# Performance work log

Hardware: AMD Instinct MI355X
Metric: run time of the kernel (lower is better)

The kernel has to match this reference:

```python
import jax, jax.numpy as jnp
import numpy as np

B, S, D = 2, 2048, 1024
H, DH = 16, 64
IGNORE = -100000.0
ATTN_SCALE = float(np.sqrt(DH))


def setup_inputs() -> dict:
    key = jax.random.key(0)
    ks = jax.random.split(key, 9)
    sc = 0.02
    return {
        "x": jax.random.normal(ks[0], (B, S, D), dtype=jnp.float32),
        "W_Q": jax.random.normal(ks[1], (H, DH, D), dtype=jnp.float32) * sc,
        "W_K": jax.random.normal(ks[2], (H, DH, D), dtype=jnp.float32) * sc,
        "W_V": jax.random.normal(ks[3], (H, DH, D), dtype=jnp.float32) * sc,
        "W_O": jax.random.normal(ks[4], (H, D, DH), dtype=jnp.float32) * sc,
        "b_Q": jax.random.normal(ks[5], (H, DH), dtype=jnp.float32) * sc,
        "b_K": jax.random.normal(ks[6], (H, DH), dtype=jnp.float32) * sc,
        "b_V": jax.random.normal(ks[7], (H, DH), dtype=jnp.float32) * sc,
        "b_O": jax.random.normal(ks[8], (D,), dtype=jnp.float32) * sc,
    }


def reference(x, W_Q, W_K, W_V, W_O, b_Q, b_K, b_V, b_O):
    # QKV projections: [b, pos, head, d_head]
    q = jnp.einsum('ihm,bpm->bpih', W_Q, x) + b_Q
    k = jnp.einsum('ihm,bpm->bpih', W_K, x) + b_K
    v = jnp.einsum('ihm,bpm->bpih', W_V, x) + b_V
    # scores[b, head, query_pos, key_pos]
    scores = jnp.einsum('bpih,bqih->bipq', q, k) / ATTN_SCALE
    Sq = x.shape[1]
    causal = jnp.tril(jnp.ones((Sq, Sq), dtype=bool))  # global causal mask
    scores = jnp.where(causal, scores, jnp.float32(IGNORE))
    attn = jax.nn.softmax(scores, axis=-1)
    # z[b, query_pos, head, d_head]
    z = jnp.einsum('bpih,biqp->bqih', v, attn)
    out = jnp.einsum('idh,bqih->bqd', W_O, z) + b_O
    return out
```

## Files before the change

kernel.cpp:

```cpp
#include <hip/hip_runtime.h>
#include <stdint.h>

typedef __attribute__((ext_vector_type(8))) short short8;
typedef __attribute__((ext_vector_type(4))) float f32x4;

#define AS1(p) ((const __attribute__((address_space(1))) void*)(p))
#define AS3(p) ((__attribute__((address_space(3))) void*)(p))

__device__ __forceinline__ void gload_lds16(const void* g, void* l) {
  __builtin_amdgcn_global_load_lds(AS1(g), AS3(l), 16, 0, 0);
}

__device__ __forceinline__ uint32_t cvtpk_bf16(float a, float b) {
  uint32_t d;
  asm("v_cvt_pk_bf16_f32 %0, %1, %2" : "=v"(d) : "v"(a), "v"(b));
  return d;
}

__device__ __forceinline__ float fast_exp2(float x) {
#if __has_builtin(__builtin_amdgcn_exp2f)
  return __builtin_amdgcn_exp2f(x);
#else
  return exp2f(x);
#endif
}

#define QSCALE 0.1803368801111244f

__global__ void prep_k(const float* __restrict__ x, const float* __restrict__ wq,
                       const float* __restrict__ wk, const float* __restrict__ wv,
                       const float* __restrict__ wo, const float* __restrict__ bq,
                       const float* __restrict__ bk, const float* __restrict__ bv,
                       uint2* __restrict__ xb, uint2* __restrict__ wqkvb,
                       uint2* __restrict__ mob, float* __restrict__ bqkv) {
  const int bid = blockIdx.x, tid = threadIdx.x;
  if (bid < 4096) {
    int i = bid * 256 + tid;
    float4 v = ((const float4*)x)[i];
    uint2 o; o.x = cvtpk_bf16(v.x, v.y); o.y = cvtpk_bf16(v.z, v.w);
    xb[i] = o;
  } else if (bid < 7168) {
    int i = (bid - 4096) * 256 + tid;
    int e = i * 4;
    const float* src = (e < (1 << 20)) ? (wq + e)
                     : (e < (2 << 20)) ? (wk + (e - (1 << 20)))
                                       : (wv + (e - (2 << 20)));
    float4 v = *(const float4*)src;
    uint2 o; o.x = cvtpk_bf16(v.x, v.y); o.y = cvtpk_bf16(v.z, v.w);
    wqkvb[i] = o;
  } else if (bid < 8192) {
    int i = (bid - 7168) * 256 + tid;
    int o4 = i * 4;
    int d = o4 >> 10, c = o4 & 1023;
    const float* s = wo + ((c >> 6) << 16) + (d << 6) + (c & 63);
    float4 v = *(const float4*)s;
    uint2 o; o.x = cvtpk_bf16(v.x, v.y); o.y = cvtpk_bf16(v.z, v.w);
    mob[i] = o;
  } else {
    int i = (bid - 8192) * 256 + tid;
    bqkv[i] = (i < 1024) ? bq[i] : (i < 2048) ? bk[i - 1024] : bv[i - 2048];
  }
}

template <int EPI>
__global__ __launch_bounds__(256) void gemm_bt(const short* __restrict__ A,
                                               const short* __restrict__ Bm,
                                               const float* __restrict__ bias,
                                               void* __restrict__ Cout, int K, int ldc) {
  __shared__ short As[128 * 64];
  __shared__ short Bs[128 * 64];
  const int t = threadIdx.x;
  const int l = t & 63, w = t >> 6;
  const int wr = w >> 1, wc = w & 1;
  const int q = l & 15, g = l >> 4;
  const long brow = (long)blockIdx.y * 128;
  const long bcol = (long)blockIdx.x * 128;
  f32x4 acc[4][4] = {};
  const int r8 = t >> 3;
  const int sc8 = (t & 7) ^ (r8 & 7);
  const short* aptr = A + (brow + r8) * (long)K + sc8 * 8;
  const short* bptr = Bm + (bcol + r8) * (long)K + sc8 * 8;
  const int qs = q & 7;
  for (int k0 = 0; k0 < K; k0 += 64) {
#pragma unroll
    for (int c = 0; c < 4; ++c) {
      gload_lds16(aptr + k0 + c * 32 * (long)K, &As[(c * 256 + t) * 8]);
      gload_lds16(bptr + k0 + c * 32 * (long)K, &Bs[(c * 256 + t) * 8]);
    }
    __syncthreads();
    short8 af[4][2], bfr[4][2];
#pragma unroll
    for (int m = 0; m < 4; ++m)
#pragma unroll
      for (int kk = 0; kk < 2; ++kk)
        af[m][kk] = *(const short8*)&As[(wr * 64 + m * 16 + q) * 64 + ((kk * 4 + g) ^ qs) * 8];
#pragma unroll
    for (int n = 0; n < 4; ++n)
#pragma unroll
      for (int kk = 0; kk < 2; ++kk)
        bfr[n][kk] = *(const short8*)&Bs[(wc * 64 + n * 16 + q) * 64 + ((kk * 4 + g) ^ qs) * 8];
#pragma unroll
    for (int m = 0; m < 4; ++m)
#pragma unroll
      for (int n = 0; n < 4; ++n) {
        acc[m][n] = __builtin_amdgcn_mfma_f32_16x16x32_bf16(af[m][0], bfr[n][0], acc[m][n], 0, 0, 0);
        acc[m][n] = __builtin_amdgcn_mfma_f32_16x16x32_bf16(af[m][1], bfr[n][1], acc[m][n], 0, 0, 0);
      }
    if (k0 + 64 < K) __syncthreads();
  }
#pragma unroll
  for (int m = 0; m < 4; ++m)
#pragma unroll
    for (int n = 0; n < 4; ++n)
#pragma unroll
      for (int r = 0; r < 4; ++r) {
        long row = brow + wr * 64 + m * 16 + g * 4 + r;
        long col = bcol + wc * 64 + n * 16 + q;
        float v = acc[m][n][r] + bias[col];
        if (EPI == 0) {
          if (col < 1024) v *= QSCALE;
          ((unsigned short*)Cout)[row * ldc + col] = (unsigned short)cvtpk_bf16(v, v);
        } else {
          ((float*)Cout)[row * ldc + col] = v;
        }
      }
}

__global__ __launch_bounds__(256) void attn(const short* __restrict__ qkv,
                                            unsigned short* __restrict__ zb) {
  __shared__ short Ks[2][64 * 64];
  __shared__ short Vt[64 * 64];
  __shared__ unsigned short Ps[8][16 * 64];
  const int bid = blockIdx.x;
  const int r_ = bid >> 7;
  const int u_ = (bid >> 3) & 15;
  const int x_ = bid & 7;
  const int bh = r_ * 8 + x_;
  const int pr = (r_ < 2) ? u_ : 15 - u_;
  const int qtA = 31 - pr, qtB = pr;
  const int b = bh >> 4, h = bh & 15;
  const int t = threadIdx.x, l = t & 63, w = t >> 6;
  const int lq = l & 15, g = l >> 4;
  const int u = t >> 3, c8 = t & 7;
  const long rowbase = (long)b * 2048;
  const short* qp = qkv + rowbase * 3072 + h * 64;
  const short* kp = qp + 1024;
  const short* vp = qp + 2048;

  short8 qfA[2], qfB[2];
#pragma unroll
  for (int kg = 0; kg < 2; ++kg) {
    qfA[kg] = *(const short8*)(qp + (long)(qtA * 64 + w * 16 + lq) * 3072 + kg * 32 + g * 8);
    qfB[kg] = *(const short8*)(qp + (long)(qtB * 64 + w * 16 + lq) * 3072 + kg * 32 + g * 8);
  }
  f32x4 zA[4] = {}, zB[4] = {};
  float mA = -1e30f, lA = 0.0f, mB = -1e30f, lB = 0.0f;

  auto step = [&](const short* ksb, unsigned short* Pw, f32x4 (&zacc)[4],
                  float& mrun, float& lrun, short8 (&qf)[2], bool diag) {
    f32x4 sacc[4] = {};
#pragma unroll
    for (int m = 0; m < 4; ++m) {
#pragma unroll
      for (int kg = 0; kg < 2; ++kg) {
        int krow = m * 16 + lq;
        int blk = kg * 4 + g;
        short8 kf = *(const short8*)&ksb[krow * 64 + (blk ^ (krow & 7)) * 8];
        sacc[m] = __builtin_amdgcn_mfma_f32_16x16x32_bf16(kf, qf[kg], sacc[m], 0, 0, 0);
      }
    }
    if (diag) {
#pragma unroll
      for (int m = 0; m < 4; ++m)
#pragma unroll
        for (int r = 0; r < 4; ++r)
          if (m * 16 + g * 4 + r > w * 16 + lq) sacc[m][r] = -1e30f;
    }
    float red[8];
#pragma unroll
    for (int i2 = 0; i2 < 8; ++i2)
      red[i2] = fmaxf(sacc[i2 >> 2][i2 & 3], sacc[2 + (i2 >> 2)][i2 & 3]);
#pragma unroll
    for (int i2 = 0; i2 < 4; ++i2) red[i2] = fmaxf(red[i2], red[i2 + 4]);
    float mx = fmaxf(fmaxf(red[0], red[2]), fmaxf(red[1], red[3]));
    mx = fmaxf(mx, __shfl_xor(mx, 16));
    mx = fmaxf(mx, __shfl_xor(mx, 32));
    if (!__all(mx <= mrun + 8.0f)) {
      float mnew = fmaxf(mrun, mx);
      float alpha = fast_exp2(mrun - mnew);
      lrun *= alpha;
#pragma unroll
      for (int r = 0; r < 4; ++r) {
        float ar = __shfl(alpha, g * 4 + r);
#pragma unroll
        for (int n2 = 0; n2 < 4; ++n2) zacc[n2][r] *= ar;
      }
      mrun = mnew;
    }
#pragma unroll
    for (int m = 0; m < 4; ++m)
#pragma unroll
      for (int r = 0; r < 4; ++r) sacc[m][r] = fast_exp2(sacc[m][r] - mrun);
    float rs[8];
#pragma unroll
    for (int i2 = 0; i2 < 8; ++i2)
      rs[i2] = sacc[i2 >> 2][i2 & 3] + sacc[2 + (i2 >> 2)][i2 & 3];
#pragma unroll
    for (int i2 = 0; i2 < 4; ++i2) rs[i2] = rs[i2] + rs[i2 + 4];
    float ts = (rs[0] + rs[2]) + (rs[1] + rs[3]);
    ts += __shfl_xor(ts, 16);
    ts += __shfl_xor(ts, 32);
    lrun += ts;
#pragma unroll
    for (int m = 0; m < 4; ++m) {
      uint2 wv;
      wv.x = cvtpk_bf16(sacc[m][0], sacc[m][1]);
      wv.y = cvtpk_bf16(sacc[m][2], sacc[m][3]);
      int c = m * 4 + g;
      int csw = c ^ ((lq & 7) << 1);
      *(uint2*)&Pw[lq * 64 + csw * 4] = wv;
    }
    short8 pf[2];
#pragma unroll
    for (int kg2 = 0; kg2 < 2; ++kg2) {
      int c0 = kg2 * 8 + g * 2;
      int c0s = c0 ^ ((lq & 7) << 1);
      pf[kg2] = *(const short8*)&Pw[lq * 64 + c0s * 4];
    }
#pragma unroll
    for (int n2 = 0; n2 < 4; ++n2) {
#pragma unroll
      for (int kg2 = 0; kg2 < 2; ++kg2) {
        int dh = n2 * 16 + lq;
        int sw = (dh & 7) ^ ((dh >> 3) & 7);
        int blk = kg2 * 4 + g;
        short8 vf = *(const short8*)&Vt[dh * 64 + ((blk ^ sw) * 8)];
        zacc[n2] = __builtin_amdgcn_mfma_f32_16x16x32_bf16(pf[kg2], vf, zacc[n2], 0, 0, 0);
      }
    }
  };

  auto stageK = [&](int tile, int buf) {
#pragma unroll
    for (int i = 0; i < 2; ++i) {
      int r = i * 32 + u;
      int cbk = (c8 ^ (r & 7)) * 8;
      gload_lds16(kp + (long)(tile * 64 + r) * 3072 + cbk, &Ks[buf][i * 2048 + t * 8]);
    }
  };

  short8 va0, va1;
  {
    stageK(0, 0);
    const short* vrow = vp + (long)(2 * u) * 3072 + c8 * 8;
    va0 = *(const short8*)vrow;
    va1 = *(const short8*)(vrow + 3072);
  }

  for (int j = 0; j <= qtA; ++j) {
    const int buf = j & 1;
    asm volatile("s_waitcnt vmcnt(0)" ::: "memory");
    __builtin_amdgcn_sched_barrier(0);
    __builtin_amdgcn_s_barrier();
    {
      int blk = u >> 2, rl = (u & 3) * 2;
#pragma unroll
      for (int idx = 0; idx < 8; ++idx) {
        int dh = c8 * 8 + idx;
        int sw = (dh & 7) ^ ((dh >> 3) & 7);
        uint32_t pk = (uint32_t)(uint16_t)va0[idx] | ((uint32_t)(uint16_t)va1[idx] << 16);
        *(uint32_t*)&Vt[dh * 64 + ((blk ^ sw) * 8) + rl] = pk;
      }
    }
    if (j < qtA) {
      stageK(j + 1, buf ^ 1);
      const short* vrow = vp + (long)((j + 1) * 64 + 2 * u) * 3072 + c8 * 8;
      va0 = *(const short8*)vrow;
      va1 = *(const short8*)(vrow + 3072);
    }
    asm volatile("s_waitcnt lgkmcnt(0)" ::: "memory");
    __builtin_amdgcn_sched_barrier(0);
    __builtin_amdgcn_s_barrier();
    step(&Ks[buf][0], &Ps[w][0], zA, mA, lA, qfA, j == qtA);
    if (j <= qtB)
      step(&Ks[buf][0], &Ps[4 + w][0], zB, mB, lB, qfB, j == qtB);
  }

  auto wout = [&](f32x4 (&zacc)[4], float lrun, int qt) {
#pragma unroll
    for (int r = 0; r < 4; ++r) {
      float linv = 1.0f / __shfl(lrun, g * 4 + r);
      long grow = rowbase + qt * 64 + w * 16 + g * 4 + r;
#pragma unroll
      for (int n2 = 0; n2 < 4; ++n2) {
        int col = h * 64 + n2 * 16 + lq;
        float zv = zacc[n2][r] * linv;
        zb[grow * 1024 + col] = (unsigned short)cvtpk_bf16(zv, zv);
      }
    }
  };
  wout(zA, lA, qtA);
  wout(zB, lB, qtB);
}

extern "C" void kernel_launch(void* const* d_in, const int* in_sizes, int n_in,
                              void* d_out, int out_size, void* d_ws, size_t ws_size,
                              hipStream_t stream) {
  const float* x  = (const float*)d_in[0];
  const float* wq = (const float*)d_in[1];
  const float* wk = (const float*)d_in[2];
  const float* wv = (const float*)d_in[3];
  const float* wo = (const float*)d_in[4];
  const float* bq = (const float*)d_in[5];
  const float* bk = (const float*)d_in[6];
  const float* bv = (const float*)d_in[7];
  const float* bo = (const float*)d_in[8];
  char* ws = (char*)d_ws;
  if (ws_size < ((size_t)48 * 1024 * 1024 + 16384)) return;
  short*          xb    = (short*)(ws);
  short*          qkvb  = (short*)(ws + ((size_t)8  << 20));
  unsigned short* zbuf  = (unsigned short*)(ws + ((size_t)32 << 20));
  short*          wqkvb = (short*)(ws + ((size_t)40 << 20));
  short*          mob   = (short*)(ws + ((size_t)46 << 20));
  float*          bqkv  = (float*)(ws + ((size_t)48 << 20));

  prep_k<<<8204, 256, 0, stream>>>(x, wq, wk, wv, wo, bq, bk, bv,
                                   (uint2*)xb, (uint2*)wqkvb, (uint2*)mob, bqkv);
  gemm_bt<0><<<dim3(24, 32), 256, 0, stream>>>(xb, wqkvb, bqkv, (void*)qkvb, 1024, 3072);
  attn      <<<512,          256, 0, stream>>>(qkvb, zbuf);
  gemm_bt<1><<<dim3(8, 32),  256, 0, stream>>>((const short*)zbuf, mob, bo, d_out, 1024, 1024);
}
```

Baseline: 110.7 us.

## Process 128-key K/V tiles per attention loop iteration instead of 64

Each iteration of the causal attention loop now stages two 64-row K and V sub-tiles (128 keys) and runs twice as many MFMAs per softmax step. The aim is to halve the number of barrier and wait points, online-softmax max/sum reductions and rescale checks per query tile. The diagonal mask now takes an offset to cover the wider tile, so some fully masked keys past the diagonal are still computed. LDS use roughly doubles and register pressure rises, which may lower occupancy.

```diff
diff --git a/kernel.cpp b/kernel.cpp
--- a/kernel.cpp
+++ b/kernel.cpp
@@ -128,9 +128,9 @@
 
 __global__ __launch_bounds__(256) void attn(const short* __restrict__ qkv,
                                             unsigned short* __restrict__ zb) {
-  __shared__ short Ks[2][64 * 64];
-  __shared__ short Vt[64 * 64];
-  __shared__ unsigned short Ps[8][16 * 64];
+  __shared__ short Ks[2][2 * 64 * 64];
+  __shared__ short Vt[2 * 64 * 64];
+  __shared__ unsigned short Ps[8][2 * 16 * 64];
   const int bid = blockIdx.x;
   const int r_ = bid >> 7;
   const int u_ = (bid >> 3) & 15;
@@ -138,6 +138,8 @@
   const int bh = r_ * 8 + x_;
   const int pr = (r_ < 2) ? u_ : 15 - u_;
   const int qtA = 31 - pr, qtB = pr;
+  const int nTA = (33 - pr) >> 1;
+  const int nTB = (qtB + 2) >> 1;
   const int b = bh >> 4, h = bh & 15;
   const int t = threadIdx.x, l = t & 63, w = t >> 6;
   const int lq = l & 15, g = l >> 4;
@@ -157,29 +159,35 @@
   float mA = -1e30f, lA = 0.0f, mB = -1e30f, lB = 0.0f;
 
   auto step = [&](const short* ksb, unsigned short* Pw, f32x4 (&zacc)[4],
-                  float& mrun, float& lrun, short8 (&qf)[2], bool diag) {
-    f32x4 sacc[4] = {};
-#pragma unroll
-    for (int m = 0; m < 4; ++m) {
+                  float& mrun, float& lrun, short8 (&qf)[2], bool diag, int dOff) {
+    f32x4 sacc[8];
+#pragma unroll
+    for (int m = 0; m < 8; ++m) {
+      sacc[m] = f32x4{0.f, 0.f, 0.f, 0.f};
+      int half = m >> 2, mh = m & 3;
+      int krow = mh * 16 + lq;
 #pragma unroll
       for (int kg = 0; kg < 2; ++kg) {
-        int krow = m * 16 + lq;
         int blk = kg * 4 + g;
-        short8 kf = *(const short8*)&ksb[krow * 64 + (blk ^ (krow & 7)) * 8];
+        short8 kf = *(const short8*)&ksb[half * 4096 + krow * 64 + (blk ^ (krow & 7)) * 8];
         sacc[m] = __builtin_amdgcn_mfma_f32_16x16x32_bf16(kf, qf[kg], sacc[m], 0, 0, 0);
       }
     }
     if (diag) {
 #pragma unroll
-      for (int m = 0; m < 4; ++m)
+      for (int m = 0; m < 8; ++m) {
+        int half = m >> 2, mh = m & 3;
 #pragma unroll
         for (int r = 0; r < 4; ++r)
-          if (m * 16 + g * 4 + r > w * 16 + lq) sacc[m][r] = -1e30f;
-    }
-    float red[8];
-#pragma unroll
-    for (int i2 = 0; i2 < 8; ++i2)
-      red[i2] = fmaxf(sacc[i2 >> 2][i2 & 3], sacc[2 + (i2 >> 2)][i2 & 3]);
+          if (half * 64 + mh * 16 + g * 4 + r > dOff + w * 16 + lq) sacc[m][r] = -1e30f;
+      }
+    }
+    float red[16];
+#pragma unroll
+    for (int i2 = 0; i2 < 16; ++i2)
+      red[i2] = fmaxf(sacc[i2 >> 2][i2 & 3], sacc[4 + (i2 >> 2)][i2 & 3]);
+#pragma unroll
+    for (int i2 = 0; i2 < 8; ++i2) red[i2] = fmaxf(red[i2], red[i2 + 8]);
 #pragma unroll
     for (int i2 = 0; i2 < 4; ++i2) red[i2] = fmaxf(red[i2], red[i2 + 4]);
     float mx = fmaxf(fmaxf(red[0], red[2]), fmaxf(red[1], red[3]));
@@ -198,13 +206,15 @@
       mrun = mnew;
     }
 #pragma unroll
-    for (int m = 0; m < 4; ++m)
+    for (int m = 0; m < 8; ++m)
 #pragma unroll
       for (int r = 0; r < 4; ++r) sacc[m][r] = fast_exp2(sacc[m][r] - mrun);
-    float rs[8];
-#pragma unroll
-    for (int i2 = 0; i2 < 8; ++i2)
-      rs[i2] = sacc[i2 >> 2][i2 & 3] + sacc[2 + (i2 >> 2)][i2 & 3];
+    float rs[16];
+#pragma unroll
+    for (int i2 = 0; i2 < 16; ++i2)
+      rs[i2] = sacc[i2 >> 2][i2 & 3] + sacc[4 + (i2 >> 2)][i2 & 3];
+#pragma unroll
+    for (int i2 = 0; i2 < 8; ++i2) rs[i2] = rs[i2] + rs[i2 + 8];
 #pragma unroll
     for (int i2 = 0; i2 < 4; ++i2) rs[i2] = rs[i2] + rs[i2 + 4];
     float ts = (rs[0] + rs[2]) + (rs[1] + rs[3]);
@@ -212,78 +222,88 @@
     ts += __shfl_xor(ts, 32);
     lrun += ts;
 #pragma unroll
-    for (int m = 0; m < 4; ++m) {
+    for (int m = 0; m < 8; ++m) {
+      int half = m >> 2, mh = m & 3;
       uint2 wv;
       wv.x = cvtpk_bf16(sacc[m][0], sacc[m][1]);
       wv.y = cvtpk_bf16(sacc[m][2], sacc[m][3]);
-      int c = m * 4 + g;
+      int c = mh * 4 + g;
       int csw = c ^ ((lq & 7) << 1);
-      *(uint2*)&Pw[lq * 64 + csw * 4] = wv;
-    }
-    short8 pf[2];
-#pragma unroll
-    for (int kg2 = 0; kg2 < 2; ++kg2) {
-      int c0 = kg2 * 8 + g * 2;
+      *(uint2*)&Pw[half * 1024 + lq * 64 + csw * 4] = wv;
+    }
+    short8 pf[4];
+#pragma unroll
+    for (int kg2 = 0; kg2 < 4; ++kg2) {
+      int half = kg2 >> 1, k2 = kg2 & 1;
+      int c0 = k2 * 8 + g * 2;
       int c0s = c0 ^ ((lq & 7) << 1);
-      pf[kg2] = *(const short8*)&Pw[lq * 64 + c0s * 4];
+      pf[kg2] = *(const short8*)&Pw[half * 1024 + lq * 64 + c0s * 4];
     }
 #pragma unroll
     for (int n2 = 0; n2 < 4; ++n2) {
 #pragma unroll
-      for (int kg2 = 0; kg2 < 2; ++kg2) {
+      for (int kg2 = 0; kg2 < 4; ++kg2) {
+        int half = kg2 >> 1;
         int dh = n2 * 16 + lq;
         int sw = (dh & 7) ^ ((dh >> 3) & 7);
-        int blk = kg2 * 4 + g;
-        short8 vf = *(const short8*)&Vt[dh * 64 + ((blk ^ sw) * 8)];
+        int blk = (kg2 & 1) * 4 + g;
+        short8 vf = *(const short8*)&Vt[half * 4096 + dh * 64 + ((blk ^ sw) * 8)];
         zacc[n2] = __builtin_amdgcn_mfma_f32_16x16x32_bf16(pf[kg2], vf, zacc[n2], 0, 0, 0);
       }
     }
   };
 
-  auto stageK = [&](int tile, int buf) {
-#pragma unroll
-    for (int i = 0; i < 2; ++i) {
-      int r = i * 32 + u;
-      int cbk = (c8 ^ (r & 7)) * 8;
-      gload_lds16(kp + (long)(tile * 64 + r) * 3072 + cbk, &Ks[buf][i * 2048 + t * 8]);
-    }
-  };
-
-  short8 va0, va1;
-  {
-    stageK(0, 0);
-    const short* vrow = vp + (long)(2 * u) * 3072 + c8 * 8;
+  short8 va0, va1, va2, va3;
+  auto stageKK = [&](int tile, int buf) {
+#pragma unroll
+    for (int hf = 0; hf < 2; ++hf)
+#pragma unroll
+      for (int i = 0; i < 2; ++i) {
+        int r = i * 32 + u;
+        int cbk = (c8 ^ (r & 7)) * 8;
+        gload_lds16(kp + ((long)tile * 128 + hf * 64 + r) * 3072 + cbk,
+                    &Ks[buf][hf * 4096 + i * 2048 + t * 8]);
+      }
+  };
+  auto loadV = [&](int tile) {
+    const short* vrow = vp + ((long)tile * 128 + 2 * u) * 3072 + c8 * 8;
     va0 = *(const short8*)vrow;
     va1 = *(const short8*)(vrow + 3072);
-  }
-
-  for (int j = 0; j <= qtA; ++j) {
-    const int buf = j & 1;
+    va2 = *(const short8*)(vrow + 64 * 3072);
+    va3 = *(const short8*)(vrow + 65 * 3072);
+  };
+  auto writeVt = [&]() {
+    int blk = u >> 2, rl = (u & 3) * 2;
+#pragma unroll
+    for (int idx = 0; idx < 8; ++idx) {
+      int dh = c8 * 8 + idx;
+      int sw = (dh & 7) ^ ((dh >> 3) & 7);
+      uint32_t p0 = (uint32_t)(uint16_t)va0[idx] | ((uint32_t)(uint16_t)va1[idx] << 16);
+      uint32_t p1 = (uint32_t)(uint16_t)va2[idx] | ((uint32_t)(uint16_t)va3[idx] << 16);
+      *(uint32_t*)&Vt[dh * 64 + ((blk ^ sw) * 8) + rl] = p0;
+      *(uint32_t*)&Vt[4096 + dh * 64 + ((blk ^ sw) * 8) + rl] = p1;
+    }
+  };
+
+  stageKK(0, 0);
+  loadV(0);
+
+  for (int jj = 0; jj < nTA; ++jj) {
+    const int buf = jj & 1;
     asm volatile("s_waitcnt vmcnt(0)" ::: "memory");
     __builtin_amdgcn_sched_barrier(0);
     __builtin_amdgcn_s_barrier();
-    {
-      int blk = u >> 2, rl = (u & 3) * 2;
-#pragma unroll
-      for (int idx = 0; idx < 8; ++idx) {
-        int dh = c8 * 8 + idx;
-        int sw = (dh & 7) ^ ((dh >> 3) & 7);
-        uint32_t pk = (uint32_t)(uint16_t)va0[idx] | ((uint32_t)(uint16_t)va1[idx] << 16);
-        *(uint32_t*)&Vt[dh * 64 + ((blk ^ sw) * 8) + rl] = pk;
-      }
-    }
-    if (j < qtA) {
-      stageK(j + 1, buf ^ 1);
-      const short* vrow = vp + (long)((j + 1) * 64 + 2 * u) * 3072 + c8 * 8;
-      va0 = *(const short8*)vrow;
-      va1 = *(const short8*)(vrow + 3072);
+    writeVt();
+    if (jj + 1 < nTA) {
+      stageKK(jj + 1, buf ^ 1);
+      loadV(jj + 1);
     }
     asm volatile("s_waitcnt lgkmcnt(0)" ::: "memory");
     __builtin_amdgcn_sched_barrier(0);
     __builtin_amdgcn_s_barrier();
-    step(&Ks[buf][0], &Ps[w][0], zA, mA, lA, qfA, j == qtA);
-    if (j <= qtB)
-      step(&Ks[buf][0], &Ps[4 + w][0], zB, mB, lB, qfB, j == qtB);
+    step(&Ks[buf][0], &Ps[w][0], zA, mA, lA, qfA, jj == nTA - 1, qtA * 64 - jj * 128);
+    if (jj < nTB)
+      step(&Ks[buf][0], &Ps[4 + w][0], zB, mB, lB, qfB, jj == nTB - 1, qtB * 64 - jj * 128);
   }
 
   auto wout = [&](f32x4 (&zacc)[4], float lrun, int qt) {
```

New measurement: 130.5 us. 17.8% more time.
